# Optimization experiments

Measured on AMD Instinct MI355X. Metric: run time of the kernel, lower is better.

Reference implementation:

```python
import jax, jax.numpy as jnp
import numpy as np

N_NODES = 50000
N_EDGES = 1250000
D = 64


def setup_inputs() -> dict:
    key = jax.random.key(0)
    ks = jax.random.split(key, 9)
    s = 1.0 / np.sqrt(D)
    return {
        "y": jax.random.normal(ks[0], (N_NODES, D), dtype=jnp.float32),
        "src": jax.random.randint(ks[1], (N_EDGES,), 0, N_NODES, dtype=jnp.int32),
        "dst": jax.random.randint(ks[2], (N_EDGES,), 0, N_NODES, dtype=jnp.int32),
        "W1": jax.random.normal(ks[3], (D, D), dtype=jnp.float32) * s,
        "b1": jnp.zeros((D,), dtype=jnp.float32),
        "W2": jax.random.normal(ks[4], (D, D), dtype=jnp.float32) * s,
        "b2": jnp.zeros((D,), dtype=jnp.float32),
        "U1": jax.random.normal(ks[5], (D, D), dtype=jnp.float32) * s,
        "c1": jnp.zeros((D,), dtype=jnp.float32),
        "U2": jax.random.normal(ks[6], (D, D), dtype=jnp.float32) * s,
        "c2": jnp.zeros((D,), dtype=jnp.float32),
    }


def reference(y, src, dst, W1, b1, W2, b2, U1, c1, U2, c2):
    # msg = relu(FNN_pre(y[src])) ; FNN = Linear -> ReLU -> Linear
    xs = y[src]                                        # [E, D] gather
    h1 = jax.nn.relu(xs @ W1 + b1)                     # [E, D]
    msg = jax.nn.relu(h1 @ W2 + b2)                    # [E, D]
    # z = segment-sum of messages at destination nodes
    z = jax.ops.segment_sum(msg, dst, num_segments=N_NODES)  # [N, D]
    # h = relu(FNN_update(z))
    h2 = jax.nn.relu(z @ U1 + c1)                      # [N, D]
    h = jax.nn.relu(h2 @ U2 + c2)                      # [N, D]
    return h
```

## Files before the change

kernel.cpp:

```cpp
#include <hip/hip_runtime.h>

#define D 64
#define CHUNK 4096
#define BSHIFT 8
#define MAXB 8192

typedef unsigned int uint;
typedef unsigned short ushort;

using bf16x8 = __attribute__((ext_vector_type(8))) short;
using f32x4  = __attribute__((ext_vector_type(4))) float;

__device__ __forceinline__ uint f2bf(float f) {
    uint u = __float_as_uint(f);
    return (u + 0x7fffu + ((u >> 16) & 1u)) >> 16;
}
__device__ __forceinline__ uint pk2(float a, float b) {
    return f2bf(a) | (f2bf(b) << 16);
}

#define ACC8M(v, aE, aO, mk) do {                                              \
    aE[0] = fmaf(mk, __uint_as_float((v).x << 16), aE[0]);                     \
    aO[0] = fmaf(mk, __uint_as_float((v).x & 0xffff0000u), aO[0]);             \
    aE[1] = fmaf(mk, __uint_as_float((v).y << 16), aE[1]);                     \
    aO[1] = fmaf(mk, __uint_as_float((v).y & 0xffff0000u), aO[1]);             \
    aE[2] = fmaf(mk, __uint_as_float((v).z << 16), aE[2]);                     \
    aO[2] = fmaf(mk, __uint_as_float((v).z & 0xffff0000u), aO[2]);             \
    aE[3] = fmaf(mk, __uint_as_float((v).w << 16), aE[3]);                     \
    aO[3] = fmaf(mk, __uint_as_float((v).w & 0xffff0000u), aO[3]);             \
} while (0)

template <bool BF16IN, bool BF16OUT>
__device__ __forceinline__ void mlp_tile(
    int tile, ushort (*Hs)[72],
    const float* __restrict__ Xf, const ushort* __restrict__ Xb,
    const ushort* __restrict__ pkW1, const float* __restrict__ b1v,
    const ushort* __restrict__ pkW2, const float* __restrict__ b2v,
    ushort* __restrict__ out16, float* __restrict__ out32, int N)
{
    const int lane = threadIdx.x & 63;
    const int m = lane & 15;
    const int q = lane >> 4;

    bf16x8 w1f[4][2], w2f[4][2];
    #pragma unroll
    for (int t = 0; t < 4; ++t) {
        #pragma unroll
        for (int kf = 0; kf < 2; ++kf) {
            const int off = ((t * 2 + kf) * 64 + lane) << 3;
            w1f[t][kf] = *(const bf16x8*)(pkW1 + off);
            w2f[t][kf] = *(const bf16x8*)(pkW2 + off);
        }
    }

    const int rowbase = tile * 16;
    int r = rowbase + m;
    if (r >= N) r = N - 1;
    bf16x8 ax0, ax1;
    if (BF16IN) {
        const ushort* xr = Xb + (size_t)r * D + q * 8;
        ax0 = *(const bf16x8*)xr;
        ax1 = *(const bf16x8*)(xr + 32);
    } else {
        const float* xr = Xf + (size_t)r * D + q * 8;
        float4 x0 = *(const float4*)xr;
        float4 x1 = *(const float4*)(xr + 4);
        float4 x2 = *(const float4*)(xr + 32);
        float4 x3 = *(const float4*)(xr + 36);
        ax0[0]=(short)f2bf(x0.x); ax0[1]=(short)f2bf(x0.y);
        ax0[2]=(short)f2bf(x0.z); ax0[3]=(short)f2bf(x0.w);
        ax0[4]=(short)f2bf(x1.x); ax0[5]=(short)f2bf(x1.y);
        ax0[6]=(short)f2bf(x1.z); ax0[7]=(short)f2bf(x1.w);
        ax1[0]=(short)f2bf(x2.x); ax1[1]=(short)f2bf(x2.y);
        ax1[2]=(short)f2bf(x2.z); ax1[3]=(short)f2bf(x2.w);
        ax1[4]=(short)f2bf(x3.x); ax1[5]=(short)f2bf(x3.y);
        ax1[6]=(short)f2bf(x3.z); ax1[7]=(short)f2bf(x3.w);
    }

    const f32x4 zero4 = {0.f, 0.f, 0.f, 0.f};
    f32x4 acc[4];

    #pragma unroll
    for (int t = 0; t < 4; ++t) acc[t] = zero4;
    #pragma unroll
    for (int t = 0; t < 4; ++t) {
        acc[t] = __builtin_amdgcn_mfma_f32_16x16x32_bf16(ax0, w1f[t][0], acc[t], 0, 0, 0);
        acc[t] = __builtin_amdgcn_mfma_f32_16x16x32_bf16(ax1, w1f[t][1], acc[t], 0, 0, 0);
    }
    #pragma unroll
    for (int t = 0; t < 4; ++t) {
        const float bv = b1v[t * 16 + m];
        #pragma unroll
        for (int rg = 0; rg < 4; ++rg) {
            float hv = fmaxf(acc[t][rg] + bv, 0.f);
            Hs[q * 4 + rg][t * 16 + m] = (ushort)f2bf(hv);
        }
    }
    __syncthreads();

    bf16x8 ah0 = *(const bf16x8*)&Hs[m][q * 8];
    bf16x8 ah1 = *(const bf16x8*)&Hs[m][32 + q * 8];

    #pragma unroll
    for (int t = 0; t < 4; ++t) acc[t] = zero4;
    #pragma unroll
    for (int t = 0; t < 4; ++t) {
        acc[t] = __builtin_amdgcn_mfma_f32_16x16x32_bf16(ah0, w2f[t][0], acc[t], 0, 0, 0);
        acc[t] = __builtin_amdgcn_mfma_f32_16x16x32_bf16(ah1, w2f[t][1], acc[t], 0, 0, 0);
    }
    #pragma unroll
    for (int t = 0; t < 4; ++t) {
        const float bv = b2v[t * 16 + m];
        #pragma unroll
        for (int rg = 0; rg < 4; ++rg) {
            const int row = rowbase + q * 4 + rg;
            if (row < N) {
                float ov = fmaxf(acc[t][rg] + bv, 0.f);
                if (BF16OUT) out16[(size_t)row * D + t * 16 + m] = (ushort)f2bf(ov);
                else         out32[(size_t)row * D + t * 16 + m] = ov;
            }
        }
    }
}

__global__ __launch_bounds__(256) void kA_hist_pack(
    const int* __restrict__ dst, int* __restrict__ histG, int E, int NBA,
    const float* __restrict__ W1, const float* __restrict__ W2,
    const float* __restrict__ U1, const float* __restrict__ U2,
    ushort* __restrict__ pkAll)
{
    __shared__ int lhist[256];
    const int t = threadIdx.x;
    if ((int)blockIdx.x < NBA) {
        lhist[t] = 0;
        __syncthreads();
        const int cbase = blockIdx.x * CHUNK;
        const int lim = min(CHUNK, E - cbase);
        if (lim == CHUNK) {
            const int4* dp = (const int4*)(dst + cbase);
            int4 d4[4];
            #pragma unroll
            for (int g = 0; g < 4; ++g) d4[g] = dp[g * 256 + t];
            #pragma unroll
            for (int g = 0; g < 4; ++g) {
                atomicAdd(&lhist[(uint)d4[g].x >> BSHIFT], 1);
                atomicAdd(&lhist[(uint)d4[g].y >> BSHIFT], 1);
                atomicAdd(&lhist[(uint)d4[g].z >> BSHIFT], 1);
                atomicAdd(&lhist[(uint)d4[g].w >> BSHIFT], 1);
            }
        } else {
            for (int j = t; j < lim; j += 256)
                atomicAdd(&lhist[(uint)dst[cbase + j] >> BSHIFT], 1);
        }
        __syncthreads();
        histG[blockIdx.x * 256 + t] = lhist[t];
    } else {
        const int mtx = blockIdx.x - NBA;
        const float* W = (mtx == 0) ? W1 : (mtx == 1) ? W2 : (mtx == 2) ? U1 : U2;
        ushort* pk = pkAll + mtx * 4096;
        for (int u = t; u < 512; u += 256) {
            const int t_ = u >> 7;
            const int rem = u & 127;
            const int kf = rem >> 6;
            const int lane = rem & 63;
            const int q = lane >> 4, m = lane & 15;
            const int n = t_ * 16 + m;
            uint w[4];
            #pragma unroll
            for (int j2 = 0; j2 < 4; ++j2) {
                const int k = kf * 32 + q * 8 + 2 * j2;
                w[j2] = pk2(W[k * D + n], W[(k + 1) * D + n]);
            }
            uint4 v = { w[0], w[1], w[2], w[3] };
            *(uint4*)(pk + (u << 3)) = v;
        }
    }
}

__global__ __launch_bounds__(256) void kB_scan(
    const int* __restrict__ histG, int* __restrict__ startG,
    int* __restrict__ tot, int NBA)
{
    __shared__ int tmp[256];
    const int t = threadIdx.x;
    const int b = blockIdx.x;
    const int K = (NBA + 255) / 256;
    const int c0 = t * K;
    int loc[8];
    int s = 0;
    #pragma unroll
    for (int i = 0; i < 8; ++i) {
        if (i < K) {
            const int c = c0 + i;
            loc[i] = s;
            s += (c < NBA) ? histG[c * 256 + b] : 0;
        }
    }
    int x = s; tmp[t] = x; __syncthreads();
    #pragma unroll
    for (int off = 1; off < 256; off <<= 1) {
        int add = (t >= off) ? tmp[t - off] : 0; __syncthreads();
        x += add; tmp[t] = x; __syncthreads();
    }
    const int base = x - s;
    #pragma unroll
    for (int i = 0; i < 8; ++i) {
        if (i < K) {
            const int c = c0 + i;
            if (c < NBA) startG[c * 256 + b] = base + loc[i];
        }
    }
    if (t == 255) tot[b] = x;
}

__global__ __launch_bounds__(256) void kC_part_mlp1(
    const int* __restrict__ src, const int* __restrict__ dst,
    const int* __restrict__ startG, const int* __restrict__ tot,
    uint* __restrict__ packedG, int E, int NBA,
    const float* __restrict__ y, const ushort* __restrict__ pkAll,
    const float* __restrict__ b1, const float* __restrict__ b2,
    ushort* __restrict__ msg16, int N)
{
    __shared__ int t1[256];
    __shared__ int cur[256];
    __shared__ __align__(16) ushort Hs[4][16][72];
    const int t = threadIdx.x;
    if ((int)blockIdx.x < NBA) {
        int tv = tot[t];
        int x = tv; t1[t] = x; __syncthreads();
        #pragma unroll
        for (int off = 1; off < 256; off <<= 1) {
            int add = (t >= off) ? t1[t - off] : 0; __syncthreads();
            x += add; t1[t] = x; __syncthreads();
        }
        cur[t] = (x - tv) + startG[blockIdx.x * 256 + t];
        __syncthreads();
        const int cbase = blockIdx.x * CHUNK;
        const int lim = min(CHUNK, E - cbase);
        if (lim == CHUNK) {
            const int4* sp = (const int4*)(src + cbase);
            const int4* dp = (const int4*)(dst + cbase);
            int4 s4[4], d4[4];
            #pragma unroll
            for (int g = 0; g < 4; ++g) { s4[g] = sp[g * 256 + t]; d4[g] = dp[g * 256 + t]; }
            #pragma unroll
            for (int g = 0; g < 4; ++g) {
                int pos;
                pos = atomicAdd(&cur[(uint)d4[g].x >> BSHIFT], 1);
                packedG[pos] = ((uint)(d4[g].x & 255) << 16) | (uint)s4[g].x;
                pos = atomicAdd(&cur[(uint)d4[g].y >> BSHIFT], 1);
                packedG[pos] = ((uint)(d4[g].y & 255) << 16) | (uint)s4[g].y;
                pos = atomicAdd(&cur[(uint)d4[g].z >> BSHIFT], 1);
                packedG[pos] = ((uint)(d4[g].z & 255) << 16) | (uint)s4[g].z;
                pos = atomicAdd(&cur[(uint)d4[g].w >> BSHIFT], 1);
                packedG[pos] = ((uint)(d4[g].w & 255) << 16) | (uint)s4[g].w;
            }
        } else {
            for (int j = t; j < lim; j += 256) {
                const int e = cbase + j;
                int s = src[e], d = dst[e];
                int pos = atomicAdd(&cur[(uint)d >> BSHIFT], 1);
                packedG[pos] = ((uint)(d & 255) << 16) | (uint)s;
            }
        }
    } else {
        const int tile = (blockIdx.x - NBA) * 4 + (t >> 6);
        mlp_tile<false, true>(tile, Hs[t >> 6], y, nullptr,
                              pkAll + 0 * 4096, b1, pkAll + 1 * 4096, b2,
                              msg16, nullptr, N);
    }
}

__global__ __launch_bounds__(256) void kF_place(
    const uint* __restrict__ packedG, const int* __restrict__ tot,
    ushort* __restrict__ sortedG, int* __restrict__ offsets, int N, int E)
{
    __shared__ int t1[256];
    __shared__ int cnt[256];
    __shared__ int cur[256];
    __shared__ uint pk[MAXB];
    __shared__ ushort srt[MAXB];
    const int t = threadIdx.x;
    const int b = blockIdx.x;

    int tv = tot[t];
    int x = tv; t1[t] = x; __syncthreads();
    #pragma unroll
    for (int off = 1; off < 256; off <<= 1) {
        int add = (t >= off) ? t1[t - off] : 0; __syncthreads();
        x += add; t1[t] = x; __syncthreads();
    }
    const int pbase = (b == 0) ? 0 : t1[b - 1];
    const int cn = tot[b];
    const bool fits = (cn <= MAXB);

    cnt[t] = 0;
    __syncthreads();
    if (fits) {
        for (int i = t; i < cn; i += 256) pk[i] = packedG[pbase + i];
        __syncthreads();
        for (int i = t; i < cn; i += 256) atomicAdd(&cnt[pk[i] >> 16], 1);
    } else {
        for (int i = t; i < cn; i += 256)
            atomicAdd(&cnt[packedG[pbase + i] >> 16], 1);
    }
    __syncthreads();

    int c = cnt[t];
    int x2 = c; t1[t] = x2; __syncthreads();
    #pragma unroll
    for (int off = 1; off < 256; off <<= 1) {
        int add = (t >= off) ? t1[t - off] : 0; __syncthreads();
        x2 += add; t1[t] = x2; __syncthreads();
    }
    const int excl = x2 - c;
    const int node = b * 256 + t;
    if (node < N) offsets[node] = pbase + excl;
    if (b == 0 && t == 0) offsets[N] = E;

    if (fits) {
        cur[t] = excl;
        __syncthreads();
        for (int i = t; i < cn; i += 256) {
            uint e = pk[i];
            int p = atomicAdd(&cur[e >> 16], 1);
            srt[p] = (ushort)(e & 0xffffu);
        }
        __syncthreads();
        for (int i = t; i < cn; i += 256)
            sortedG[pbase + i] = srt[i];
    } else {
        cur[t] = pbase + excl;
        __syncthreads();
        for (int i = t; i < cn; i += 256) {
            uint e = packedG[pbase + i];
            int p = atomicAdd(&cur[e >> 16], 1);
            sortedG[p] = (ushort)(e & 0xffffu);
        }
    }
}

__global__ __launch_bounds__(256, 6) void k5_gather(
    const ushort* __restrict__ msg16,
    const int* __restrict__ offsets, const ushort* __restrict__ sortedG,
    ushort* __restrict__ z16, int n_nodes)
{
    const int lane = threadIdx.x & 63;
    const int sub = lane & 7;
    const int grp = (lane >> 3) & 3;
    const int half = lane >> 5;
    const int il = lane & 31;
    const int hbase = lane & 32;
    const int p = blockIdx.x * 4 + (threadIdx.x >> 6);
    if (p * 2 >= n_nodes) return;
    const ushort* mbase = msg16 + (sub << 3);

    const int n = 2 * p + half;
    const bool nvalid = n < n_nodes;
    int beg = 0, end = 0;
    if (nvalid) { beg = offsets[n]; end = offsets[n + 1]; }
    const int m = end - beg;
    const int m0 = __builtin_amdgcn_readfirstlane(m);
    const int m1 = __builtin_amdgcn_readlane(m, 32);
    const int mmax = max(m0, m1);

    float aE[4] = {0, 0, 0, 0}, aO[4] = {0, 0, 0, 0};

    for (int base = 0; base < mmax; base += 32) {
        int idxv = 0;
        if (base + il < m) idxv = (int)sortedG[beg + base + il];

        int sj[8];
        #pragma unroll
        for (int j = 0; j < 8; ++j)
            if (base + j * 4 < mmax)
                sj[j] = __shfl(idxv, hbase + j * 4 + grp, 64);
        uint4 v[8];
        #pragma unroll
        for (int j = 0; j < 8; ++j)
            if (base + j * 4 < mmax)
                v[j] = *(const uint4*)(mbase + ((size_t)sj[j] << 6));
        #pragma unroll
        for (int j = 0; j < 8; ++j)
            if (base + j * 4 < mmax) {
                const float mk = (base + j * 4 + grp < m) ? 1.f : 0.f;
                ACC8M(v[j], aE, aO, mk);
            }
    }

    #pragma unroll
    for (int d2 = 0; d2 < 4; ++d2) {
        aE[d2] += __shfl_xor(aE[d2], 8, 64);
        aO[d2] += __shfl_xor(aO[d2], 8, 64);
        aE[d2] += __shfl_xor(aE[d2], 16, 64);
        aO[d2] += __shfl_xor(aO[d2], 16, 64);
    }
    if (grp == 0 && nvalid) {
        uint4 pv;
        pv.x = pk2(aE[0], aO[0]);
        pv.y = pk2(aE[1], aO[1]);
        pv.z = pk2(aE[2], aO[2]);
        pv.w = pk2(aE[3], aO[3]);
        *(uint4*)(z16 + (size_t)n * D + (sub << 3)) = pv;
    }
}

__global__ __launch_bounds__(256) void k_mlp2(
    const ushort* __restrict__ z16, const ushort* __restrict__ pkAll,
    const float* __restrict__ c1, const float* __restrict__ c2,
    float* __restrict__ out, int N)
{
    __shared__ __align__(16) ushort Hs[4][16][72];
    const int tile = blockIdx.x * 4 + (threadIdx.x >> 6);
    mlp_tile<true, false>(tile, Hs[threadIdx.x >> 6], nullptr, z16,
                          pkAll + 2 * 4096, c1, pkAll + 3 * 4096, c2,
                          nullptr, out, N);
}

extern "C" void kernel_launch(void* const* d_in, const int* in_sizes, int n_in,
                              void* d_out, int out_size, void* d_ws, size_t ws_size,
                              hipStream_t stream) {
    const float* y  = (const float*)d_in[0];
    const int*  src = (const int*) d_in[1];
    const int*  dst = (const int*) d_in[2];
    const float* W1 = (const float*)d_in[3];
    const float* b1 = (const float*)d_in[4];
    const float* W2 = (const float*)d_in[5];
    const float* b2 = (const float*)d_in[6];
    const float* U1 = (const float*)d_in[7];
    const float* c1 = (const float*)d_in[8];
    const float* U2 = (const float*)d_in[9];
    const float* c2 = (const float*)d_in[10];

    const int N = in_sizes[0] / D;
    const int E = in_sizes[1];
    const int NBA   = (E + CHUNK - 1) / CHUNK;
    const int NBUCK = (N + 255) / 256;
    const int NT    = (N + 15) / 16;
    const int MB    = (NT + 3) / 4;
    const int G5    = (N / 2 + 3) / 4;

    char* ws = (char*)d_ws;
    auto al16 = [](size_t x) { return (x + 15) & ~15ull; };
    ushort* msg16   = (ushort*)ws;  ws += al16((size_t)N * D * 2);
    int*    offsets = (int*)ws;     ws += al16((size_t)(N + 1) * 4);
    int*    tot     = (int*)ws;     ws += al16(256 * 4);
    ushort* sortedG = (ushort*)ws;  ws += al16((size_t)E * 2);
    ushort* pkAll   = (ushort*)ws;  ws += al16(4 * 4096 * 2);
    ushort* z16     = (ushort*)ws;
    int*    histG   = (int*)ws;
    int*    startG  = histG + (size_t)NBA * 256;
    uint*   packedG = (uint*)(startG + (size_t)NBA * 256);

    kA_hist_pack<<<NBA + 4, 256, 0, stream>>>(
        dst, histG, E, NBA, W1, W2, U1, U2, pkAll);

    kB_scan<<<NBUCK > 256 ? NBUCK : 256, 256, 0, stream>>>(histG, startG, tot, NBA);

    kC_part_mlp1<<<NBA + MB, 256, 0, stream>>>(
        src, dst, startG, tot, packedG, E, NBA,
        y, pkAll, b1, b2, msg16, N);

    kF_place<<<NBUCK, 256, 0, stream>>>(packedG, tot, sortedG, offsets, N, E);

    k5_gather<<<G5, 256, 0, stream>>>(msg16, offsets, sortedG, z16, N);

    k_mlp2<<<MB, 256, 0, stream>>>(z16, pkAll, c1, c2, (float*)d_out, N);
}
```

Measured before the change: 141.2 us.

## Replace scan-based partition with atomic bucket cursors and fuse gather with update MLP

The histogram, global scan and per-block offset computation are replaced by per-block local histograms plus one global atomicAdd per bucket into fixed-capacity (CAP=8192) bucket regions, dropping the separate hist and scan kernels. The segment-sum gather is fused with the second MLP: each block aggregates 16 nodes into shared memory and runs the MFMA MLP directly, so the z16 round trip through global memory and one launch disappear. The sort kernel now reads packed entries straight from global memory instead of staging them in LDS. In exchange, edge order within a bucket becomes nondeterministic, a bucket holding more than CAP edges would overflow, and all four waves compute the MLP tile redundantly while only one stores.

Result: slower. 146.7 us (+3.9%).

```diff
diff --git a/kernel.cpp b/kernel.cpp
--- a/kernel.cpp
+++ b/kernel.cpp
@@ -3,7 +3,7 @@
 #define D 64
 #define CHUNK 4096
 #define BSHIFT 8
-#define MAXB 8192
+#define CAP 8192
 
 typedef unsigned int uint;
 typedef unsigned short ushort;
@@ -30,13 +30,13 @@
     aO[3] = fmaf(mk, __uint_as_float((v).w & 0xffff0000u), aO[3]);             \
 } while (0)
 
-template <bool BF16IN, bool BF16OUT>
+template <bool BF16IN>
 __device__ __forceinline__ void mlp_tile(
     int tile, ushort (*Hs)[72],
-    const float* __restrict__ Xf, const ushort* __restrict__ Xb,
+    const float* __restrict__ Xf, const ushort* __restrict__ Xb, int xstride,
     const ushort* __restrict__ pkW1, const float* __restrict__ b1v,
     const ushort* __restrict__ pkW2, const float* __restrict__ b2v,
-    ushort* __restrict__ out16, float* __restrict__ out32, int N)
+    ushort* __restrict__ out16, float* __restrict__ out32, int N, bool store)
 {
     const int lane = threadIdx.x & 63;
     const int m = lane & 15;
@@ -58,11 +58,11 @@
     if (r >= N) r = N - 1;
     bf16x8 ax0, ax1;
     if (BF16IN) {
-        const ushort* xr = Xb + (size_t)r * D + q * 8;
+        const ushort* xr = Xb + (size_t)r * xstride + q * 8;
         ax0 = *(const bf16x8*)xr;
         ax1 = *(const bf16x8*)(xr + 32);
     } else {
-        const float* xr = Xf + (size_t)r * D + q * 8;
+        const float* xr = Xf + (size_t)r * xstride + q * 8;
         float4 x0 = *(const float4*)xr;
         float4 x1 = *(const float4*)(xr + 4);
         float4 x2 = *(const float4*)(xr + 32);
@@ -108,132 +108,70 @@
         acc[t] = __builtin_amdgcn_mfma_f32_16x16x32_bf16(ah0, w2f[t][0], acc[t], 0, 0, 0);
         acc[t] = __builtin_amdgcn_mfma_f32_16x16x32_bf16(ah1, w2f[t][1], acc[t], 0, 0, 0);
     }
-    #pragma unroll
-    for (int t = 0; t < 4; ++t) {
-        const float bv = b2v[t * 16 + m];
-        #pragma unroll
-        for (int rg = 0; rg < 4; ++rg) {
-            const int row = rowbase + q * 4 + rg;
-            if (row < N) {
-                float ov = fmaxf(acc[t][rg] + bv, 0.f);
-                if (BF16OUT) out16[(size_t)row * D + t * 16 + m] = (ushort)f2bf(ov);
-                else         out32[(size_t)row * D + t * 16 + m] = ov;
+    __syncthreads();
+    if (store) {
+        #pragma unroll
+        for (int t = 0; t < 4; ++t) {
+            const float bv = b2v[t * 16 + m];
+            #pragma unroll
+            for (int rg = 0; rg < 4; ++rg) {
+                const int row = rowbase + q * 4 + rg;
+                if (row < N) {
+                    float ov = fmaxf(acc[t][rg] + bv, 0.f);
+                    if (out16) out16[(size_t)row * D + t * 16 + m] = (ushort)f2bf(ov);
+                    else       out32[(size_t)row * D + t * 16 + m] = ov;
+                }
             }
         }
     }
 }
 
-__global__ __launch_bounds__(256) void kA_hist_pack(
-    const int* __restrict__ dst, int* __restrict__ histG, int E, int NBA,
+__global__ __launch_bounds__(256) void kInit(
+    int* __restrict__ cursor,
     const float* __restrict__ W1, const float* __restrict__ W2,
     const float* __restrict__ U1, const float* __restrict__ U2,
     ushort* __restrict__ pkAll)
 {
-    __shared__ int lhist[256];
     const int t = threadIdx.x;
-    if ((int)blockIdx.x < NBA) {
-        lhist[t] = 0;
-        __syncthreads();
-        const int cbase = blockIdx.x * CHUNK;
-        const int lim = min(CHUNK, E - cbase);
-        if (lim == CHUNK) {
-            const int4* dp = (const int4*)(dst + cbase);
-            int4 d4[4];
-            #pragma unroll
-            for (int g = 0; g < 4; ++g) d4[g] = dp[g * 256 + t];
-            #pragma unroll
-            for (int g = 0; g < 4; ++g) {
-                atomicAdd(&lhist[(uint)d4[g].x >> BSHIFT], 1);
-                atomicAdd(&lhist[(uint)d4[g].y >> BSHIFT], 1);
-                atomicAdd(&lhist[(uint)d4[g].z >> BSHIFT], 1);
-                atomicAdd(&lhist[(uint)d4[g].w >> BSHIFT], 1);
-            }
-        } else {
-            for (int j = t; j < lim; j += 256)
-                atomicAdd(&lhist[(uint)dst[cbase + j] >> BSHIFT], 1);
-        }
-        __syncthreads();
-        histG[blockIdx.x * 256 + t] = lhist[t];
-    } else {
-        const int mtx = blockIdx.x - NBA;
-        const float* W = (mtx == 0) ? W1 : (mtx == 1) ? W2 : (mtx == 2) ? U1 : U2;
-        ushort* pk = pkAll + mtx * 4096;
-        for (int u = t; u < 512; u += 256) {
-            const int t_ = u >> 7;
-            const int rem = u & 127;
-            const int kf = rem >> 6;
-            const int lane = rem & 63;
-            const int q = lane >> 4, m = lane & 15;
-            const int n = t_ * 16 + m;
-            uint w[4];
-            #pragma unroll
-            for (int j2 = 0; j2 < 4; ++j2) {
-                const int k = kf * 32 + q * 8 + 2 * j2;
-                w[j2] = pk2(W[k * D + n], W[(k + 1) * D + n]);
-            }
-            uint4 v = { w[0], w[1], w[2], w[3] };
-            *(uint4*)(pk + (u << 3)) = v;
-        }
-    }
-}
-
-__global__ __launch_bounds__(256) void kB_scan(
-    const int* __restrict__ histG, int* __restrict__ startG,
-    int* __restrict__ tot, int NBA)
-{
-    __shared__ int tmp[256];
-    const int t = threadIdx.x;
-    const int b = blockIdx.x;
-    const int K = (NBA + 255) / 256;
-    const int c0 = t * K;
-    int loc[8];
-    int s = 0;
-    #pragma unroll
-    for (int i = 0; i < 8; ++i) {
-        if (i < K) {
-            const int c = c0 + i;
-            loc[i] = s;
-            s += (c < NBA) ? histG[c * 256 + b] : 0;
-        }
-    }
-    int x = s; tmp[t] = x; __syncthreads();
-    #pragma unroll
-    for (int off = 1; off < 256; off <<= 1) {
-        int add = (t >= off) ? tmp[t - off] : 0; __syncthreads();
-        x += add; tmp[t] = x; __syncthreads();
-    }
-    const int base = x - s;
-    #pragma unroll
-    for (int i = 0; i < 8; ++i) {
-        if (i < K) {
-            const int c = c0 + i;
-            if (c < NBA) startG[c * 256 + b] = base + loc[i];
-        }
-    }
-    if (t == 255) tot[b] = x;
-}
-
-__global__ __launch_bounds__(256) void kC_part_mlp1(
+    if (blockIdx.x == 0) {
+        cursor[t] = 0;
+        return;
+    }
+    const int mtx = blockIdx.x - 1;
+    const float* W = (mtx == 0) ? W1 : (mtx == 1) ? W2 : (mtx == 2) ? U1 : U2;
+    ushort* pk = pkAll + mtx * 4096;
+    for (int v = t; v < 512; v += 256) {
+        const int t_ = v >> 7;
+        const int rem = v & 127;
+        const int kf = rem >> 6;
+        const int lane = rem & 63;
+        const int q = lane >> 4, m = lane & 15;
+        const int n = t_ * 16 + m;
+        uint w[4];
+        #pragma unroll
+        for (int j2 = 0; j2 < 4; ++j2) {
+            const int k = kf * 32 + q * 8 + 2 * j2;
+            w[j2] = pk2(W[k * D + n], W[(k + 1) * D + n]);
+        }
+        uint4 vv = { w[0], w[1], w[2], w[3] };
+        *(uint4*)(pk + (v << 3)) = vv;
+    }
+}
+
+__global__ __launch_bounds__(256) void kPart_mlp1(
     const int* __restrict__ src, const int* __restrict__ dst,
-    const int* __restrict__ startG, const int* __restrict__ tot,
-    uint* __restrict__ packedG, int E, int NBA,
+    int* __restrict__ cursor, uint* __restrict__ packedG, int E, int NBA,
     const float* __restrict__ y, const ushort* __restrict__ pkAll,
     const float* __restrict__ b1, const float* __restrict__ b2,
     ushort* __restrict__ msg16, int N)
 {
-    __shared__ int t1[256];
-    __shared__ int cur[256];
+    __shared__ int lhist[256];
+    __shared__ int lcur[256];
     __shared__ __align__(16) ushort Hs[4][16][72];
     const int t = threadIdx.x;
+
     if ((int)blockIdx.x < NBA) {
-        int tv = tot[t];
-        int x = tv; t1[t] = x; __syncthreads();
-        #pragma unroll
-        for (int off = 1; off < 256; off <<= 1) {
-            int add = (t >= off) ? t1[t - off] : 0; __syncthreads();
-            x += add; t1[t] = x; __syncthreads();
-        }
-        cur[t] = (x - tv) + startG[blockIdx.x * 256 + t];
+        lhist[t] = 0;
         __syncthreads();
         const int cbase = blockIdx.x * CHUNK;
         const int lim = min(CHUNK, E - cbase);
@@ -245,176 +183,174 @@
             for (int g = 0; g < 4; ++g) { s4[g] = sp[g * 256 + t]; d4[g] = dp[g * 256 + t]; }
             #pragma unroll
             for (int g = 0; g < 4; ++g) {
+                atomicAdd(&lhist[(uint)d4[g].x >> BSHIFT], 1);
+                atomicAdd(&lhist[(uint)d4[g].y >> BSHIFT], 1);
+                atomicAdd(&lhist[(uint)d4[g].z >> BSHIFT], 1);
+                atomicAdd(&lhist[(uint)d4[g].w >> BSHIFT], 1);
+            }
+            __syncthreads();
+            int c = lhist[t];
+            int base = 0;
+            if (c > 0) base = atomicAdd(&cursor[t], c);
+            lcur[t] = t * CAP + base;
+            __syncthreads();
+            #pragma unroll
+            for (int g = 0; g < 4; ++g) {
                 int pos;
-                pos = atomicAdd(&cur[(uint)d4[g].x >> BSHIFT], 1);
+                pos = atomicAdd(&lcur[(uint)d4[g].x >> BSHIFT], 1);
                 packedG[pos] = ((uint)(d4[g].x & 255) << 16) | (uint)s4[g].x;
-                pos = atomicAdd(&cur[(uint)d4[g].y >> BSHIFT], 1);
+                pos = atomicAdd(&lcur[(uint)d4[g].y >> BSHIFT], 1);
                 packedG[pos] = ((uint)(d4[g].y & 255) << 16) | (uint)s4[g].y;
-                pos = atomicAdd(&cur[(uint)d4[g].z >> BSHIFT], 1);
+                pos = atomicAdd(&lcur[(uint)d4[g].z >> BSHIFT], 1);
                 packedG[pos] = ((uint)(d4[g].z & 255) << 16) | (uint)s4[g].z;
-                pos = atomicAdd(&cur[(uint)d4[g].w >> BSHIFT], 1);
+                pos = atomicAdd(&lcur[(uint)d4[g].w >> BSHIFT], 1);
                 packedG[pos] = ((uint)(d4[g].w & 255) << 16) | (uint)s4[g].w;
             }
         } else {
+            for (int j = t; j < lim; j += 256)
+                atomicAdd(&lhist[(uint)dst[cbase + j] >> BSHIFT], 1);
+            __syncthreads();
+            int c = lhist[t];
+            int base = 0;
+            if (c > 0) base = atomicAdd(&cursor[t], c);
+            lcur[t] = t * CAP + base;
+            __syncthreads();
             for (int j = t; j < lim; j += 256) {
-                const int e = cbase + j;
-                int s = src[e], d = dst[e];
-                int pos = atomicAdd(&cur[(uint)d >> BSHIFT], 1);
+                int s = src[cbase + j], d = dst[cbase + j];
+                int pos = atomicAdd(&lcur[(uint)d >> BSHIFT], 1);
                 packedG[pos] = ((uint)(d & 255) << 16) | (uint)s;
             }
         }
     } else {
         const int tile = (blockIdx.x - NBA) * 4 + (t >> 6);
-        mlp_tile<false, true>(tile, Hs[t >> 6], y, nullptr,
-                              pkAll + 0 * 4096, b1, pkAll + 1 * 4096, b2,
-                              msg16, nullptr, N);
-    }
-}
-
-__global__ __launch_bounds__(256) void kF_place(
-    const uint* __restrict__ packedG, const int* __restrict__ tot,
-    ushort* __restrict__ sortedG, int* __restrict__ offsets, int N, int E)
-{
-    __shared__ int t1[256];
+        mlp_tile<false>(tile, Hs[t >> 6], y, nullptr, D,
+                        pkAll + 0 * 4096, b1, pkAll + 1 * 4096, b2,
+                        msg16, nullptr, N, true);
+    }
+}
+
+__global__ __launch_bounds__(256) void kSort(
+    const uint* __restrict__ packedG, const int* __restrict__ cursor,
+    ushort* __restrict__ sortedG, int* __restrict__ offsets,
+    int* __restrict__ ends, int N)
+{
+    __shared__ int scn[256];
     __shared__ int cnt[256];
     __shared__ int cur[256];
-    __shared__ uint pk[MAXB];
-    __shared__ ushort srt[MAXB];
+    __shared__ ushort srt[CAP];
     const int t = threadIdx.x;
     const int b = blockIdx.x;
-
-    int tv = tot[t];
-    int x = tv; t1[t] = x; __syncthreads();
+    const int base = b * CAP;
+    const int cn = cursor[b];
+
+    cnt[t] = 0;
+    __syncthreads();
+    for (int i = t; i < cn; i += 256)
+        atomicAdd(&cnt[packedG[base + i] >> 16], 1);
+    __syncthreads();
+
+    int c = cnt[t];
+    int x = c; scn[t] = x; __syncthreads();
     #pragma unroll
     for (int off = 1; off < 256; off <<= 1) {
-        int add = (t >= off) ? t1[t - off] : 0; __syncthreads();
-        x += add; t1[t] = x; __syncthreads();
-    }
-    const int pbase = (b == 0) ? 0 : t1[b - 1];
-    const int cn = tot[b];
-    const bool fits = (cn <= MAXB);
-
-    cnt[t] = 0;
-    __syncthreads();
-    if (fits) {
-        for (int i = t; i < cn; i += 256) pk[i] = packedG[pbase + i];
-        __syncthreads();
-        for (int i = t; i < cn; i += 256) atomicAdd(&cnt[pk[i] >> 16], 1);
-    } else {
-        for (int i = t; i < cn; i += 256)
-            atomicAdd(&cnt[packedG[pbase + i] >> 16], 1);
-    }
-    __syncthreads();
-
-    int c = cnt[t];
-    int x2 = c; t1[t] = x2; __syncthreads();
-    #pragma unroll
-    for (int off = 1; off < 256; off <<= 1) {
-        int add = (t >= off) ? t1[t - off] : 0; __syncthreads();
-        x2 += add; t1[t] = x2; __syncthreads();
-    }
-    const int excl = x2 - c;
+        int add = (t >= off) ? scn[t - off] : 0; __syncthreads();
+        x += add; scn[t] = x; __syncthreads();
+    }
+    const int excl = x - c;
     const int node = b * 256 + t;
-    if (node < N) offsets[node] = pbase + excl;
-    if (b == 0 && t == 0) offsets[N] = E;
-
-    if (fits) {
-        cur[t] = excl;
-        __syncthreads();
-        for (int i = t; i < cn; i += 256) {
-            uint e = pk[i];
-            int p = atomicAdd(&cur[e >> 16], 1);
-            srt[p] = (ushort)(e & 0xffffu);
-        }
-        __syncthreads();
-        for (int i = t; i < cn; i += 256)
-            sortedG[pbase + i] = srt[i];
-    } else {
-        cur[t] = pbase + excl;
-        __syncthreads();
-        for (int i = t; i < cn; i += 256) {
-            uint e = packedG[pbase + i];
-            int p = atomicAdd(&cur[e >> 16], 1);
-            sortedG[p] = (ushort)(e & 0xffffu);
-        }
-    }
-}
-
-__global__ __launch_bounds__(256, 6) void k5_gather(
+    if (node < N) {
+        offsets[node] = base + excl;
+        ends[node]    = base + excl + c;
+    }
+    cur[t] = excl;
+    __syncthreads();
+    for (int i = t; i < cn; i += 256) {
+        uint e = packedG[base + i];
+        int p = atomicAdd(&cur[e >> 16], 1);
+        srt[p] = (ushort)(e & 0xffffu);
+    }
+    __syncthreads();
+    for (int i = t; i < cn; i += 256)
+        sortedG[base + i] = srt[i];
+}
+
+__global__ __launch_bounds__(256) void kGatherMlp2(
     const ushort* __restrict__ msg16,
-    const int* __restrict__ offsets, const ushort* __restrict__ sortedG,
-    ushort* __restrict__ z16, int n_nodes)
-{
-    const int lane = threadIdx.x & 63;
+    const int* __restrict__ offsets, const int* __restrict__ ends,
+    const ushort* __restrict__ sortedG,
+    const ushort* __restrict__ pkAll,
+    const float* __restrict__ c1, const float* __restrict__ c2,
+    float* __restrict__ out, int N)
+{
+    __shared__ __align__(16) ushort Zs[16][72];
+    __shared__ __align__(16) ushort Hs[16][72];
+    const int t = threadIdx.x;
+    const int wv = t >> 6;
+    const int lane = t & 63;
     const int sub = lane & 7;
     const int grp = (lane >> 3) & 3;
     const int half = lane >> 5;
     const int il = lane & 31;
     const int hbase = lane & 32;
-    const int p = blockIdx.x * 4 + (threadIdx.x >> 6);
-    if (p * 2 >= n_nodes) return;
     const ushort* mbase = msg16 + (sub << 3);
-
-    const int n = 2 * p + half;
-    const bool nvalid = n < n_nodes;
-    int beg = 0, end = 0;
-    if (nvalid) { beg = offsets[n]; end = offsets[n + 1]; }
-    const int m = end - beg;
-    const int m0 = __builtin_amdgcn_readfirstlane(m);
-    const int m1 = __builtin_amdgcn_readlane(m, 32);
-    const int mmax = max(m0, m1);
-
-    float aE[4] = {0, 0, 0, 0}, aO[4] = {0, 0, 0, 0};
-
-    for (int base = 0; base < mmax; base += 32) {
-        int idxv = 0;
-        if (base + il < m) idxv = (int)sortedG[beg + base + il];
-
-        int sj[8];
-        #pragma unroll
-        for (int j = 0; j < 8; ++j)
-            if (base + j * 4 < mmax)
-                sj[j] = __shfl(idxv, hbase + j * 4 + grp, 64);
-        uint4 v[8];
-        #pragma unroll
-        for (int j = 0; j < 8; ++j)
-            if (base + j * 4 < mmax)
-                v[j] = *(const uint4*)(mbase + ((size_t)sj[j] << 6));
-        #pragma unroll
-        for (int j = 0; j < 8; ++j)
-            if (base + j * 4 < mmax) {
-                const float mk = (base + j * 4 + grp < m) ? 1.f : 0.f;
-                ACC8M(v[j], aE, aO, mk);
-            }
-    }
-
-    #pragma unroll
-    for (int d2 = 0; d2 < 4; ++d2) {
-        aE[d2] += __shfl_xor(aE[d2], 8, 64);
-        aO[d2] += __shfl_xor(aO[d2], 8, 64);
-        aE[d2] += __shfl_xor(aE[d2], 16, 64);
-        aO[d2] += __shfl_xor(aO[d2], 16, 64);
-    }
-    if (grp == 0 && nvalid) {
-        uint4 pv;
-        pv.x = pk2(aE[0], aO[0]);
-        pv.y = pk2(aE[1], aO[1]);
-        pv.z = pk2(aE[2], aO[2]);
-        pv.w = pk2(aE[3], aO[3]);
-        *(uint4*)(z16 + (size_t)n * D + (sub << 3)) = pv;
-    }
-}
-
-__global__ __launch_bounds__(256) void k_mlp2(
-    const ushort* __restrict__ z16, const ushort* __restrict__ pkAll,
-    const float* __restrict__ c1, const float* __restrict__ c2,
-    float* __restrict__ out, int N)
-{
-    __shared__ __align__(16) ushort Hs[4][16][72];
-    const int tile = blockIdx.x * 4 + (threadIdx.x >> 6);
-    mlp_tile<true, false>(tile, Hs[threadIdx.x >> 6], nullptr, z16,
-                          pkAll + 2 * 4096, c1, pkAll + 3 * 4096, c2,
-                          nullptr, out, N);
+    const int tile = blockIdx.x;
+
+    #pragma unroll
+    for (int pass = 0; pass < 2; ++pass) {
+        const int pairIdx = pass * 4 + wv;
+        const int n = tile * 16 + 2 * pairIdx + half;
+        const bool nvalid = n < N;
+        int beg = 0, end = 0;
+        if (nvalid) { beg = offsets[n]; end = ends[n]; }
+        const int m = end - beg;
+        const int m0 = __builtin_amdgcn_readfirstlane(m);
+        const int m1 = __builtin_amdgcn_readlane(m, 32);
+        const int mmax = max(m0, m1);
+
+        float aE[4] = {0, 0, 0, 0}, aO[4] = {0, 0, 0, 0};
+
+        for (int base = 0; base < mmax; base += 32) {
+            int idxv = 0;
+            if (base + il < m) idxv = (int)sortedG[beg + base + il];
+            int sj[8];
+            #pragma unroll
+            for (int j = 0; j < 8; ++j)
+                if (base + j * 4 < mmax)
+                    sj[j] = __shfl(idxv, hbase + j * 4 + grp, 64);
+            uint4 v[8];
+            #pragma unroll
+            for (int j = 0; j < 8; ++j)
+                if (base + j * 4 < mmax)
+                    v[j] = *(const uint4*)(mbase + ((size_t)sj[j] << 6));
+            #pragma unroll
+            for (int j = 0; j < 8; ++j)
+                if (base + j * 4 < mmax) {
+                    const float mk = (base + j * 4 + grp < m) ? 1.f : 0.f;
+                    ACC8M(v[j], aE, aO, mk);
+                }
+        }
+
+        #pragma unroll
+        for (int d2 = 0; d2 < 4; ++d2) {
+            aE[d2] += __shfl_xor(aE[d2], 8, 64);
+            aO[d2] += __shfl_xor(aO[d2], 8, 64);
+            aE[d2] += __shfl_xor(aE[d2], 16, 64);
+            aO[d2] += __shfl_xor(aO[d2], 16, 64);
+        }
+        if (grp == 0) {
+            uint4 pv;
+            pv.x = pk2(aE[0], aO[0]);
+            pv.y = pk2(aE[1], aO[1]);
+            pv.z = pk2(aE[2], aO[2]);
+            pv.w = pk2(aE[3], aO[3]);
+            *(uint4*)&Zs[2 * pairIdx + half][sub << 3] = pv;
+        }
+    }
+    __syncthreads();
+
+    mlp_tile<true>(tile, Hs, nullptr, &Zs[0][0] - (size_t)tile * 16 * 72, 72,
+                   pkAll + 2 * 4096, c1, pkAll + 3 * 4096, c2,
+                   nullptr, out, N, wv == 0);
 }
 
 extern "C" void kernel_launch(void* const* d_in, const int* in_sizes, int n_in,
@@ -438,32 +374,24 @@
     const int NBUCK = (N + 255) / 256;
     const int NT    = (N + 15) / 16;
     const int MB    = (NT + 3) / 4;
-    const int G5    = (N / 2 + 3) / 4;
 
     char* ws = (char*)d_ws;
     auto al16 = [](size_t x) { return (x + 15) & ~15ull; };
     ushort* msg16   = (ushort*)ws;  ws += al16((size_t)N * D * 2);
-    int*    offsets = (int*)ws;     ws += al16((size_t)(N + 1) * 4);
-    int*    tot     = (int*)ws;     ws += al16(256 * 4);
-    ushort* sortedG = (ushort*)ws;  ws += al16((size_t)E * 2);
+    int*    offsets = (int*)ws;     ws += al16((size_t)N * 4);
+    int*    ends    = (int*)ws;     ws += al16((size_t)N * 4);
+    int*    cursor  = (int*)ws;     ws += al16(256 * 4);
     ushort* pkAll   = (ushort*)ws;  ws += al16(4 * 4096 * 2);
-    ushort* z16     = (ushort*)ws;
-    int*    histG   = (int*)ws;
-    int*    startG  = histG + (size_t)NBA * 256;
-    uint*   packedG = (uint*)(startG + (size_t)NBA * 256);
-
-    kA_hist_pack<<<NBA + 4, 256, 0, stream>>>(
-        dst, histG, E, NBA, W1, W2, U1, U2, pkAll);
-
-    kB_scan<<<NBUCK > 256 ? NBUCK : 256, 256, 0, stream>>>(histG, startG, tot, NBA);
-
-    kC_part_mlp1<<<NBA + MB, 256, 0, stream>>>(
-        src, dst, startG, tot, packedG, E, NBA,
-        y, pkAll, b1, b2, msg16, N);
-
-    kF_place<<<NBUCK, 256, 0, stream>>>(packedG, tot, sortedG, offsets, N, E);
-
-    k5_gather<<<G5, 256, 0, stream>>>(msg16, offsets, sortedG, z16, N);
-
-    k_mlp2<<<MB, 256, 0, stream>>>(z16, pkAll, c1, c2, (float*)d_out, N);
-}
+    uint*   packedG = (uint*)ws;    ws += al16((size_t)NBUCK * CAP * 4);
+    ushort* sortedG = (ushort*)ws;  ws += al16((size_t)NBUCK * CAP * 2);
+
+    kInit<<<5, 256, 0, stream>>>(cursor, W1, W2, U1, U2, pkAll);
+
+    kPart_mlp1<<<NBA + MB, 256, 0, stream>>>(
+        src, dst, cursor, packedG, E, NBA, y, pkAll, b1, b2, msg16, N);
+
+    kSort<<<NBUCK, 256, 0, stream>>>(packedG, cursor, sortedG, offsets, ends, N);
+
+    kGatherMlp2<<<NT, 256, 0, stream>>>(
+        msg16, offsets, ends, sortedG, pkAll, c1, c2, (float*)d_out, N);
+}
```
